# Kernel optimization log

Measured on AMD Instinct MI355X. Metric: run time of the kernel, lower is better.

The kernel has to match this reference:

```python
import jax, jax.numpy as jnp
import numpy as np

HEADS = 8

def setup_inputs() -> dict:
    key = jax.random.key(0)
    ks = jax.random.split(key, 4)
    b, n, d = 4, 4097, 128  # n = 64*64 + 1 (CLS + spatial)
    x = jax.random.normal(ks[0], (b, n, d), dtype=jnp.float32)
    W_qkv = jax.random.normal(ks[1], (d, 3 * d), dtype=jnp.float32) * (d ** -0.5)
    b_qkv = jnp.zeros((3 * d,), dtype=jnp.float32)
    W_out = jax.random.normal(ks[2], (d, d), dtype=jnp.float32) * (d ** -0.5)
    b_out = jnp.zeros((d,), dtype=jnp.float32)
    return {"x": x, "W_qkv": W_qkv, "b_qkv": b_qkv, "W_out": W_out, "b_out": b_out}

def reference(x, W_qkv, b_qkv, W_out, b_out):
    b, n, d = x.shape
    h = HEADS
    dh = d // h
    scale = d ** -0.5  # note: module scales by dim**-0.5, not head_dim**-0.5
    qkv = x @ W_qkv + b_qkv                      # [b, n, 3d]
    q, k, v = jnp.split(qkv, 3, axis=-1)
    def to_heads(t):
        return t.reshape(b, n, h, dh).transpose(0, 2, 1, 3)  # [b, h, n, dh]
    q, k, v = to_heads(q), to_heads(k), to_heads(v)
    dots = jnp.einsum('bhid,bhjd->bhij', q, k) * scale       # [b, h, n, n]
    attn = jax.nn.softmax(dots, axis=-1)
    out = jnp.einsum('bhij,bhjd->bhid', attn, v)             # [b, h, n, dh]
    out = out.transpose(0, 2, 1, 3).reshape(b, n, d)
    return out @ W_out + b_out
```

## Files before the change

### kernel.cpp

```cpp
#include <hip/hip_runtime.h>
#include <hip/hip_bf16.h>
#include <stdint.h>


#define BB 4
#define NN 4097
#define NNP 4112
#define DD 128
#define HH 8
#define DH 16
#define BH (BB*HH)
#define ROWS (BB*NN)
#define MT  1025

typedef _Float16 h4 __attribute__((ext_vector_type(4)));
typedef _Float16 h8 __attribute__((ext_vector_type(8)));
typedef __fp16   fp16v2 __attribute__((ext_vector_type(2)));
typedef float    f4 __attribute__((ext_vector_type(4)));

#define QSCALE (0.08838834764831845f * 1.4426950408889634f)

#if __has_builtin(__builtin_amdgcn_exp2f)
#define EXP2F(x) __builtin_amdgcn_exp2f(x)
#else
#define EXP2F(x) exp2f(x)
#endif

union H4u { h4 v; fp16v2 p[2]; };

static __device__ __forceinline__ H4u pack4u(float a, float b, float c, float d) {
    H4u u;
#if __has_builtin(__builtin_amdgcn_cvt_pkrtz)
    u.p[0] = __builtin_amdgcn_cvt_pkrtz(a, b);
    u.p[1] = __builtin_amdgcn_cvt_pkrtz(c, d);
#else
    u.v[0] = (_Float16)a; u.v[1] = (_Float16)b; u.v[2] = (_Float16)c; u.v[3] = (_Float16)d;
#endif
    return u;
}

__global__ __launch_bounds__(256) void prep(
    const float* __restrict__ x,
    const float* __restrict__ Wqkv,
    const float* __restrict__ Wout,
    _Float16* __restrict__ x16,
    _Float16* __restrict__ WqkvT,
    _Float16* __restrict__ WoutT)
{
    const int id = blockIdx.x*256 + threadIdx.x;
    const int NX8 = ROWS*DD/8;
    if (id < NX8) {
        const float4* s = (const float4*)(x + (size_t)id*8);
        const float4 a = s[0], b = s[1];
        const H4u u0 = pack4u(a.x, a.y, a.z, a.w);
        const H4u u1 = pack4u(b.x, b.y, b.z, b.w);
        h4* d = (h4*)(x16 + (size_t)id*8);
        d[0] = u0.v; d[1] = u1.v;
    } else if (id < NX8 + 384*128) {
        const int e = id - NX8;
        const int n = e >> 7, k = e & 127;
        const float s = (n < 128) ? QSCALE : 1.0f;
        WqkvT[e] = (_Float16)(Wqkv[k*384 + n] * s);
    } else if (id < NX8 + 384*128 + 128*128) {
        const int e = id - NX8 - 384*128;
        const int n = e >> 7, k = e & 127;
        WoutT[e] = (_Float16)(Wout[k*128 + n]);
    }
}

__global__ __launch_bounds__(256) void qkv_mfma(
    const _Float16* __restrict__ x16,
    const _Float16* __restrict__ WqkvT,
    const float* __restrict__ bqkv,
    _Float16* __restrict__ Qh,
    _Float16* __restrict__ Kh,
    _Float16* __restrict__ Vh)
{
    const int wid  = blockIdx.x*4 + (threadIdx.x >> 6);
    if (wid >= MT) return;
    const int lane = threadIdx.x & 63;
    const int quad = lane >> 4, l16 = lane & 15;

    const int arow = wid*16 + l16;
    const int arc  = (arow < ROWS) ? arow : (ROWS - 1);
    h4 af[8];
    #pragma unroll
    for (int kk = 0; kk < 8; ++kk)
        af[kk] = *(const h4*)(x16 + (size_t)arc*DD + kk*16 + quad*4);

    const int r0 = wid*16 + quad*4;

    for (int nt = 0; nt < 24; nt += 2) {
        const float b0 = bqkv[nt*16 + l16]      * ((nt   < 8) ? QSCALE : 1.0f);
        const float b1 = bqkv[nt*16 + 16 + l16] * ((nt+1 < 8) ? QSCALE : 1.0f);
        f4 a0 = {b0,b0,b0,b0}, a1 = {b1,b1,b1,b1};
        #pragma unroll
        for (int kk = 0; kk < 8; ++kk) {
            const h4 bf0 = *(const h4*)(WqkvT + (size_t)(nt*16     + l16)*DD + kk*16 + quad*4);
            const h4 bf1 = *(const h4*)(WqkvT + (size_t)(nt*16 + 16 + l16)*DD + kk*16 + quad*4);
            a0 = __builtin_amdgcn_mfma_f32_16x16x16f16(af[kk], bf0, a0, 0, 0, 0);
            a1 = __builtin_amdgcn_mfma_f32_16x16x16f16(af[kk], bf1, a1, 0, 0, 0);
        }
        #pragma unroll
        for (int u = 0; u < 2; ++u) {
            const int ntc = nt + u;
            const int which = ntc >> 3, head = ntc & 7;
            _Float16* base = (which == 0) ? Qh : ((which == 1) ? Kh : Vh);
            const f4 av = u ? a1 : a0;
            #pragma unroll
            for (int r = 0; r < 4; ++r) {
                const int row = r0 + r;
                if (row < ROWS) {
                    const int bidx = row / NN;
                    const int nrow = row - bidx*NN;
                    base[((size_t)(bidx*HH + head)*NNP + nrow)*DH + l16] = (_Float16)av[r];
                }
            }
        }
    }
}

__global__ __launch_bounds__(256) void vt_transpose(
    const _Float16* __restrict__ Vh,
    _Float16* __restrict__ Vt)
{
    __shared__ _Float16 tile[128][DH + 2];
    const int tl  = blockIdx.x;
    const int bh  = blockIdx.y;
    const int tid = threadIdx.x;
    const int n0  = tl * 128;
    const int rem = (n0 + 128 <= NNP) ? 128 : (NNP - n0);

    {
        const int r  = tid >> 1;
        const int i8 = (tid & 1) * 8;
        const int rc = (r < rem) ? r : (rem - 1);
        const h8 v = *(const h8*)(Vh + ((size_t)bh*NNP + n0 + rc)*DH + i8);
        #pragma unroll
        for (int j = 0; j < 8; ++j) tile[r][i8 + j] = v[j];
    }
    __syncthreads();
    {
        const int i    = tid >> 4;
        const int nseg = tid & 15;
        if (nseg * 8 < rem) {
            h8 v;
            #pragma unroll
            for (int j = 0; j < 8; ++j) v[j] = tile[nseg*8 + j][i];
            *(h8*)(Vt + ((size_t)bh*DH + i)*NNP + n0 + nseg*8) = v;
        }
    }
}

__global__ __launch_bounds__(256, 8) void attn_mfma(
    const _Float16* __restrict__ Qh,
    const _Float16* __restrict__ Kh,
    const _Float16* __restrict__ Vt,
    _Float16* __restrict__ PACC,
    float* __restrict__ PL)
{
    const int qt   = blockIdx.x;
    const int bh   = blockIdx.y;
    const int sp   = blockIdx.z;
    const int tid  = threadIdx.x;
    const int wave = tid >> 6;
    const int lane = tid & 63;
    const int quad = lane >> 4;
    const int l16  = lane & 15;
    const int bidx = bh >> 3, head = bh & 7;

    const int qbase = qt*256 + wave*64;

    const _Float16* Qb = Qh + (size_t)bh*NNP*DH;
    h4 qf[4];
    #pragma unroll
    for (int g = 0; g < 4; ++g) {
        const int qr = qbase + g*16 + l16;
        const int qc = (qr < NN) ? qr : (NN-1);
        qf[g] = *(const h4*)(Qb + (size_t)qc*DH + quad*4);
    }

    f4 acc[4] = {{0,0,0,0},{0,0,0,0},{0,0,0,0},{0,0,0,0}};
    float ls[4] = {0.f,0.f,0.f,0.f};

    const int t0 = sp*64;
    const int t1 = t0 + 64;

    const _Float16* kp = Kh + ((size_t)bh*NNP + (size_t)t0*16 + l16)*DH + quad*4;
    const _Float16* vp = Vt + ((size_t)bh*DH + l16)*NNP + t0*16 + quad*4;

    h4 ak = *(const h4*)kp;
    h4 av = *(const h4*)vp;
    const f4 zero = {0.f,0.f,0.f,0.f};
#if __has_builtin(__builtin_amdgcn_fdot2)
    const fp16v2 one2 = {(__fp16)1.0f, (__fp16)1.0f};
#endif

    for (int tt = t0; tt < t1; ++tt) {
        kp += 16*DH; vp += 16;
        const h4 nak = *(const h4*)kp;
        const h4 nav = *(const h4*)vp;
        #pragma unroll
        for (int g = 0; g < 4; ++g) {
            f4 d = __builtin_amdgcn_mfma_f32_16x16x16f16(ak, qf[g], zero, 0, 0, 0);
            const float p0 = EXP2F(d[0]), p1 = EXP2F(d[1]), p2 = EXP2F(d[2]), p3 = EXP2F(d[3]);
            const H4u pb = pack4u(p0, p1, p2, p3);
#if __has_builtin(__builtin_amdgcn_fdot2)
            ls[g] = __builtin_amdgcn_fdot2(pb.p[0], one2,
                     __builtin_amdgcn_fdot2(pb.p[1], one2, ls[g], false), false);
#else
            ls[g] += (p0 + p1) + (p2 + p3);
#endif
            acc[g] = __builtin_amdgcn_mfma_f32_16x16x16f16(av, pb.v, acc[g], 0, 0, 0);
        }
        ak = nak; av = nav;
    }

    if (sp == 3) {
        #pragma unroll
        for (int g = 0; g < 4; ++g) {
            f4 d = __builtin_amdgcn_mfma_f32_16x16x16f16(ak, qf[g], zero, 0, 0, 0);
            const float p0 = (quad == 0) ? EXP2F(d[0]) : 0.f;
            ls[g] += p0;
            const H4u pb = pack4u(p0, 0.f, 0.f, 0.f);
            acc[g] = __builtin_amdgcn_mfma_f32_16x16x16f16(av, pb.v, acc[g], 0, 0, 0);
        }
    }

    const size_t rb = (size_t)sp*ROWS + (size_t)bidx*NN;
    #pragma unroll
    for (int g = 0; g < 4; ++g) {
        float l = ls[g];
        l += __shfl_xor(l, 16);
        l += __shfl_xor(l, 32);
        const int qr = qbase + g*16 + l16;
        if (qr < NN) {
            const float inv = 1.0f / l;
            const H4u st = pack4u(acc[g][0]*inv, acc[g][1]*inv, acc[g][2]*inv, acc[g][3]*inv);
            *(h4*)(PACC + (rb + qr)*DD + head*DH + quad*4) = st.v;
            if (quad == 0) PL[(rb + qr)*HH + head] = l;
        }
    }
}

__global__ __launch_bounds__(256) void out_mfma(
    const _Float16* __restrict__ PACC,
    const float* __restrict__ PL,
    const _Float16* __restrict__ WoutT,
    const float* __restrict__ bout,
    float* __restrict__ out)
{
    const int wid  = blockIdx.x*4 + (threadIdx.x >> 6);
    if (wid >= MT) return;
    const int lane = threadIdx.x & 63;
    const int quad = lane >> 4, l16 = lane & 15;

    const int arow = wid*16 + l16;
    const int arc  = (arow < ROWS) ? arow : (ROWS - 1);

    h4 af[8];
    #pragma unroll
    for (int kk = 0; kk < 8; ++kk) {
        float n0 = 0.f, n1 = 0.f, n2 = 0.f, n3 = 0.f, lsum = 0.f;
        #pragma unroll
        for (int sp = 0; sp < 4; ++sp) {
            const float l = PL[((size_t)sp*ROWS + arc)*HH + kk];
            lsum += l;
            const h4 p = *(const h4*)(PACC + ((size_t)sp*ROWS + arc)*DD + kk*16 + quad*4);
            n0 += l*(float)p[0]; n1 += l*(float)p[1];
            n2 += l*(float)p[2]; n3 += l*(float)p[3];
        }
        const float inv = 1.0f / lsum;
        const H4u u = pack4u(n0*inv, n1*inv, n2*inv, n3*inv);
        af[kk] = u.v;
    }

    const int r0 = wid*16 + quad*4;

    for (int nt = 0; nt < 8; nt += 2) {
        const float b0 = bout[nt*16 + l16];
        const float b1 = bout[nt*16 + 16 + l16];
        f4 a0 = {b0,b0,b0,b0}, a1 = {b1,b1,b1,b1};
        #pragma unroll
        for (int kk = 0; kk < 8; ++kk) {
            const h4 bf0 = *(const h4*)(WoutT + (size_t)(nt*16      + l16)*DD + kk*16 + quad*4);
            const h4 bf1 = *(const h4*)(WoutT + (size_t)(nt*16 + 16 + l16)*DD + kk*16 + quad*4);
            a0 = __builtin_amdgcn_mfma_f32_16x16x16f16(af[kk], bf0, a0, 0, 0, 0);
            a1 = __builtin_amdgcn_mfma_f32_16x16x16f16(af[kk], bf1, a1, 0, 0, 0);
        }
        #pragma unroll
        for (int r = 0; r < 4; ++r) {
            const int row = r0 + r;
            if (row < ROWS) {
                out[(size_t)row*DD + nt*16      + l16] = a0[r];
                out[(size_t)row*DD + nt*16 + 16 + l16] = a1[r];
            }
        }
    }
}

extern "C" void kernel_launch(void* const* d_in, const int* in_sizes, int n_in,
                              void* d_out, int out_size, void* d_ws, size_t ws_size,
                              hipStream_t stream) {
    const float* x    = (const float*)d_in[0];
    const float* Wqkv = (const float*)d_in[1];
    const float* bqkv = (const float*)d_in[2];
    const float* Wout = (const float*)d_in[3];
    const float* bout = (const float*)d_in[4];
    for (int i = 0; i < n_in; ++i) {
        switch (in_sizes[i]) {
            case 2097664: x    = (const float*)d_in[i]; break;
            case 49152:   Wqkv = (const float*)d_in[i]; break;
            case 384:     bqkv = (const float*)d_in[i]; break;
            case 16384:   Wout = (const float*)d_in[i]; break;
            case 128:     bout = (const float*)d_in[i]; break;
            default: break;
        }
    }
    float* out = (float*)d_out;

    const size_t perh = (size_t)BH * NNP * DH;
    _Float16* Qh   = (_Float16*)d_ws;
    _Float16* Kh   = Qh + perh;
    _Float16* Vt   = Kh + perh;
    _Float16* Vh   = Vt + perh;
    _Float16* PACC = Vh;
    _Float16* x16  = Vh + perh;
    float*    PL    = (float*)(PACC + (size_t)4*ROWS*DD);
    _Float16* WqkvT = (_Float16*)(PL + (size_t)4*ROWS*HH);
    _Float16* WoutT = WqkvT + 384*128;

    const int NX8 = ROWS*DD/8;
    const int prep_total = NX8 + 384*128 + 128*128;

    hipLaunchKernelGGL(prep, dim3((prep_total + 255)/256), dim3(256), 0, stream,
                       x, Wqkv, Wout, x16, WqkvT, WoutT);
    hipLaunchKernelGGL(qkv_mfma, dim3((MT + 3)/4), dim3(256), 0, stream,
                       x16, WqkvT, bqkv, Qh, Kh, Vh);
    hipLaunchKernelGGL(vt_transpose, dim3(33, BH), dim3(256), 0, stream,
                       Vh, Vt);
    hipLaunchKernelGGL(attn_mfma, dim3(17, BH, 4), dim3(256), 0, stream,
                       Qh, Kh, Vt, PACC, PL);
    hipLaunchKernelGGL(out_mfma, dim3((MT + 3)/4), dim3(256), 0, stream,
                       PACC, PL, WoutT, bout, out);
}
```

Measured before the change: 195.5 us.

## Fuse fp16 prep and V transpose into QKV projection, split N across blocks

Removes the separate prep and vt_transpose kernels. The QKV projection now reads fp32 x and Wqkv directly and converts them to fp16 in registers. It stages the outputs in LDS, writes Q and K with vectorized stores, and writes V already transposed. The QKV and output projections also gain a second grid dimension that splits the output columns across blocks, which raises parallelism. The cost is repeated fp32 weight loads and conversions in every wave, plus scalar strided Vt stores, in exchange for two fewer launches and less intermediate global traffic.

```diff
diff --git a/kernel.cpp b/kernel.cpp
--- a/kernel.cpp
+++ b/kernel.cpp
@@ -39,115 +39,98 @@
     return u;
 }
 
-__global__ __launch_bounds__(256) void prep(
+__global__ __launch_bounds__(256) void qkv_mfma(
     const float* __restrict__ x,
     const float* __restrict__ Wqkv,
-    const float* __restrict__ Wout,
-    _Float16* __restrict__ x16,
-    _Float16* __restrict__ WqkvT,
-    _Float16* __restrict__ WoutT)
-{
-    const int id = blockIdx.x*256 + threadIdx.x;
-    const int NX8 = ROWS*DD/8;
-    if (id < NX8) {
-        const float4* s = (const float4*)(x + (size_t)id*8);
-        const float4 a = s[0], b = s[1];
-        const H4u u0 = pack4u(a.x, a.y, a.z, a.w);
-        const H4u u1 = pack4u(b.x, b.y, b.z, b.w);
-        h4* d = (h4*)(x16 + (size_t)id*8);
-        d[0] = u0.v; d[1] = u1.v;
-    } else if (id < NX8 + 384*128) {
-        const int e = id - NX8;
-        const int n = e >> 7, k = e & 127;
-        const float s = (n < 128) ? QSCALE : 1.0f;
-        WqkvT[e] = (_Float16)(Wqkv[k*384 + n] * s);
-    } else if (id < NX8 + 384*128 + 128*128) {
-        const int e = id - NX8 - 384*128;
-        const int n = e >> 7, k = e & 127;
-        WoutT[e] = (_Float16)(Wout[k*128 + n]);
-    }
-}
-
-__global__ __launch_bounds__(256) void qkv_mfma(
-    const _Float16* __restrict__ x16,
-    const _Float16* __restrict__ WqkvT,
     const float* __restrict__ bqkv,
     _Float16* __restrict__ Qh,
     _Float16* __restrict__ Kh,
-    _Float16* __restrict__ Vh)
-{
-    const int wid  = blockIdx.x*4 + (threadIdx.x >> 6);
-    if (wid >= MT) return;
-    const int lane = threadIdx.x & 63;
-    const int quad = lane >> 4, l16 = lane & 15;
-
-    const int arow = wid*16 + l16;
-    const int arc  = (arow < ROWS) ? arow : (ROWS - 1);
-    h4 af[8];
-    #pragma unroll
-    for (int kk = 0; kk < 8; ++kk)
-        af[kk] = *(const h4*)(x16 + (size_t)arc*DD + kk*16 + quad*4);
-
-    const int r0 = wid*16 + quad*4;
-
-    for (int nt = 0; nt < 24; nt += 2) {
-        const float b0 = bqkv[nt*16 + l16]      * ((nt   < 8) ? QSCALE : 1.0f);
-        const float b1 = bqkv[nt*16 + 16 + l16] * ((nt+1 < 8) ? QSCALE : 1.0f);
-        f4 a0 = {b0,b0,b0,b0}, a1 = {b1,b1,b1,b1};
-        #pragma unroll
-        for (int kk = 0; kk < 8; ++kk) {
-            const h4 bf0 = *(const h4*)(WqkvT + (size_t)(nt*16     + l16)*DD + kk*16 + quad*4);
-            const h4 bf1 = *(const h4*)(WqkvT + (size_t)(nt*16 + 16 + l16)*DD + kk*16 + quad*4);
-            a0 = __builtin_amdgcn_mfma_f32_16x16x16f16(af[kk], bf0, a0, 0, 0, 0);
-            a1 = __builtin_amdgcn_mfma_f32_16x16x16f16(af[kk], bf1, a1, 0, 0, 0);
-        }
-        #pragma unroll
-        for (int u = 0; u < 2; ++u) {
-            const int ntc = nt + u;
-            const int which = ntc >> 3, head = ntc & 7;
-            _Float16* base = (which == 0) ? Qh : ((which == 1) ? Kh : Vh);
-            const f4 av = u ? a1 : a0;
-            #pragma unroll
-            for (int r = 0; r < 4; ++r) {
-                const int row = r0 + r;
-                if (row < ROWS) {
-                    const int bidx = row / NN;
-                    const int nrow = row - bidx*NN;
-                    base[((size_t)(bidx*HH + head)*NNP + nrow)*DH + l16] = (_Float16)av[r];
-                }
-            }
-        }
-    }
-}
-
-__global__ __launch_bounds__(256) void vt_transpose(
-    const _Float16* __restrict__ Vh,
     _Float16* __restrict__ Vt)
 {
-    __shared__ _Float16 tile[128][DH + 2];
-    const int tl  = blockIdx.x;
-    const int bh  = blockIdx.y;
-    const int tid = threadIdx.x;
-    const int n0  = tl * 128;
-    const int rem = (n0 + 128 <= NNP) ? 128 : (NNP - n0);
-
-    {
-        const int r  = tid >> 1;
-        const int i8 = (tid & 1) * 8;
-        const int rc = (r < rem) ? r : (rem - 1);
-        const h8 v = *(const h8*)(Vh + ((size_t)bh*NNP + n0 + rc)*DH + i8);
-        #pragma unroll
-        for (int j = 0; j < 8; ++j) tile[r][i8 + j] = v[j];
+    __shared__ _Float16 lds[4][12][16][24];
+
+    const int tid  = threadIdx.x;
+    const int w    = tid >> 6;
+    const int lane = tid & 63;
+    const int quad = lane >> 4, l16 = lane & 15;
+    const int nsel = blockIdx.y;
+    const int wid  = blockIdx.x*4 + w;
+    const int widc = (wid < MT) ? wid : (MT-1);
+    const int arow = widc*16 + l16;
+    const int arc  = (arow < ROWS) ? arow : (ROWS-1);
+
+    h4 af[8];
+    #pragma unroll
+    for (int kk = 0; kk < 8; ++kk) {
+        const float4 xv = *(const float4*)(x + (size_t)arc*DD + kk*16 + quad*4);
+        af[kk] = pack4u(xv.x, xv.y, xv.z, xv.w).v;
+    }
+
+    f4 acc[12];
+    #pragma unroll
+    for (int ntl = 0; ntl < 12; ++ntl) {
+        const int ntc = nsel*12 + ntl;
+        const float b = bqkv[ntc*16 + l16] * ((ntc < 8) ? QSCALE : 1.0f);
+        acc[ntl] = (f4){b, b, b, b};
+    }
+
+    #pragma unroll
+    for (int kk = 0; kk < 8; ++kk) {
+        const int kb = kk*16 + quad*4;
+        const float* Wr = Wqkv + (size_t)kb*384 + nsel*192 + l16;
+        #pragma unroll
+        for (int ntl = 0; ntl < 12; ++ntl) {
+            const float w0 = Wr[ntl*16];
+            const float w1 = Wr[384  + ntl*16];
+            const float w2 = Wr[768  + ntl*16];
+            const float w3 = Wr[1152 + ntl*16];
+            const float sc = ((nsel*12 + ntl) < 8) ? QSCALE : 1.0f;
+            acc[ntl] = __builtin_amdgcn_mfma_f32_16x16x16f16(
+                af[kk], pack4u(w0*sc, w1*sc, w2*sc, w3*sc).v, acc[ntl], 0, 0, 0);
+        }
+    }
+
+    #pragma unroll
+    for (int ntl = 0; ntl < 12; ++ntl) {
+        #pragma unroll
+        for (int r = 0; r < 4; ++r)
+            lds[w][ntl][quad*4 + r][l16] = (_Float16)acc[ntl][r];
     }
     __syncthreads();
-    {
-        const int i    = tid >> 4;
-        const int nseg = tid & 15;
-        if (nseg * 8 < rem) {
-            h8 v;
+
+    const int ntqk = (nsel == 0) ? 12 : 4;
+    for (int u = tid; u < 4*ntqk*32; u += 256) {
+        const int w2  = u / (ntqk*32);
+        const int rem = u - w2*(ntqk*32);
+        const int ntl = rem >> 5;
+        const int j   = rem & 31;
+        const int ntc = nsel*12 + ntl;
+        const int head = ntc & 7;
+        const int row = (blockIdx.x*4 + w2)*16 + (j >> 1);
+        if (row >= ROWS) continue;
+        const int bidx = row / NN;
+        const int nrow = row - bidx*NN;
+        _Float16* base = ((ntc >> 3) == 0) ? Qh : Kh;
+        const h8 v = *(const h8*)&lds[w2][ntl][j >> 1][(j & 1)*8];
+        *(h8*)(base + ((size_t)(bidx*HH + head)*NNP + nrow)*DH + (j & 1)*8) = v;
+    }
+
+    if (nsel == 1) {
+        for (int u = tid; u < 512; u += 256) {
+            const int w2   = u >> 7;
+            const int rem  = u & 127;
+            const int ntl  = 4 + (rem >> 4);
+            const int c    = rem & 15;
+            const int head = ntl - 4;
+            const int row0 = (blockIdx.x*4 + w2)*16;
             #pragma unroll
-            for (int j = 0; j < 8; ++j) v[j] = tile[nseg*8 + j][i];
-            *(h8*)(Vt + ((size_t)bh*DH + i)*NNP + n0 + nseg*8) = v;
+            for (int rr = 0; rr < 16; ++rr) {
+                const int row = row0 + rr;
+                if (row >= ROWS) break;
+                const int bidx = row / NN;
+                const int nrow = row - bidx*NN;
+                Vt[((size_t)(bidx*HH + head)*DH + c)*NNP + nrow] = lds[w2][ntl][rr][c];
+            }
         }
     }
 }
@@ -246,7 +229,7 @@
 __global__ __launch_bounds__(256) void out_mfma(
     const _Float16* __restrict__ PACC,
     const float* __restrict__ PL,
-    const _Float16* __restrict__ WoutT,
+    const float* __restrict__ Wout,
     const float* __restrict__ bout,
     float* __restrict__ out)
 {
@@ -254,6 +237,7 @@
     if (wid >= MT) return;
     const int lane = threadIdx.x & 63;
     const int quad = lane >> 4, l16 = lane & 15;
+    const int nsel = blockIdx.y;
 
     const int arow = wid*16 + l16;
     const int arc  = (arow < ROWS) ? arow : (ROWS - 1);
@@ -271,20 +255,21 @@
             n2 += l*(float)p[2]; n3 += l*(float)p[3];
         }
         const float inv = 1.0f / lsum;
-        const H4u u = pack4u(n0*inv, n1*inv, n2*inv, n3*inv);
-        af[kk] = u.v;
+        af[kk] = pack4u(n0*inv, n1*inv, n2*inv, n3*inv).v;
     }
 
     const int r0 = wid*16 + quad*4;
 
-    for (int nt = 0; nt < 8; nt += 2) {
+    for (int nt = nsel*4; nt < nsel*4 + 4; nt += 2) {
         const float b0 = bout[nt*16 + l16];
         const float b1 = bout[nt*16 + 16 + l16];
         f4 a0 = {b0,b0,b0,b0}, a1 = {b1,b1,b1,b1};
         #pragma unroll
         for (int kk = 0; kk < 8; ++kk) {
-            const h4 bf0 = *(const h4*)(WoutT + (size_t)(nt*16      + l16)*DD + kk*16 + quad*4);
-            const h4 bf1 = *(const h4*)(WoutT + (size_t)(nt*16 + 16 + l16)*DD + kk*16 + quad*4);
+            const int kb = kk*16 + quad*4;
+            const float* Wr = Wout + (size_t)kb*DD + nt*16 + l16;
+            const h4 bf0 = pack4u(Wr[0],      Wr[DD],      Wr[2*DD],      Wr[3*DD]).v;
+            const h4 bf1 = pack4u(Wr[16],     Wr[DD+16],   Wr[2*DD+16],   Wr[3*DD+16]).v;
             a0 = __builtin_amdgcn_mfma_f32_16x16x16f16(af[kk], bf0, a0, 0, 0, 0);
             a1 = __builtin_amdgcn_mfma_f32_16x16x16f16(af[kk], bf1, a1, 0, 0, 0);
         }
@@ -323,24 +308,13 @@
     _Float16* Qh   = (_Float16*)d_ws;
     _Float16* Kh   = Qh + perh;
     _Float16* Vt   = Kh + perh;
-    _Float16* Vh   = Vt + perh;
-    _Float16* PACC = Vh;
-    _Float16* x16  = Vh + perh;
-    float*    PL    = (float*)(PACC + (size_t)4*ROWS*DD);
-    _Float16* WqkvT = (_Float16*)(PL + (size_t)4*ROWS*HH);
-    _Float16* WoutT = WqkvT + 384*128;
-
-    const int NX8 = ROWS*DD/8;
-    const int prep_total = NX8 + 384*128 + 128*128;
-
-    hipLaunchKernelGGL(prep, dim3((prep_total + 255)/256), dim3(256), 0, stream,
-                       x, Wqkv, Wout, x16, WqkvT, WoutT);
-    hipLaunchKernelGGL(qkv_mfma, dim3((MT + 3)/4), dim3(256), 0, stream,
-                       x16, WqkvT, bqkv, Qh, Kh, Vh);
-    hipLaunchKernelGGL(vt_transpose, dim3(33, BH), dim3(256), 0, stream,
-                       Vh, Vt);
+    _Float16* PACC = Vt + perh;
+    float*    PL   = (float*)(PACC + (size_t)4*ROWS*DD);
+
+    hipLaunchKernelGGL(qkv_mfma, dim3((MT + 3)/4, 2), dim3(256), 0, stream,
+                       x, Wqkv, bqkv, Qh, Kh, Vt);
     hipLaunchKernelGGL(attn_mfma, dim3(17, BH, 4), dim3(256), 0, stream,
                        Qh, Kh, Vt, PACC, PL);
-    hipLaunchKernelGGL(out_mfma, dim3((MT + 3)/4), dim3(256), 0, stream,
-                       PACC, PL, WoutT, bout, out);
-}
+    hipLaunchKernelGGL(out_mfma, dim3((MT + 3)/4, 2), dim3(256), 0, stream,
+                       PACC, PL, Wout, bout, out);
+}
```

Result: no change. 196.4 us (+0.4%).
